# Optimization experiments

Measured on AMD Instinct MI355X. Metric: run time of the kernel, lower is better.

## Reference

```python
import jax, jax.numpy as jnp
import numpy as np

B, S, H = 8, 32, 2048          # batch, block (query) length, hidden size
NH, NKV, HD = 16, 2, 128       # attention heads, kv heads, head_dim
KV_LEN = 8192                  # block kv-cache length
GROUPS = NH // NKV
SCALE = HD ** -0.5


def rotate_half(x):
    x1, x2 = jnp.split(x, 2, axis=-1)
    return jnp.concatenate((-x2, x1), axis=-1)


def setup_inputs() -> dict:
    key = jax.random.key(0)
    ks = jax.random.split(key, 12)
    inv_freq = 1.0 / (10000.0 ** (jnp.arange(0, HD, 2, dtype=jnp.float32) / HD))
    pos = jnp.arange(S, dtype=jnp.float32)[:, None] * inv_freq[None, :]  # [S, HD/2]
    ang = jnp.concatenate([pos, pos], axis=-1)                           # [S, HD]
    cos = jnp.broadcast_to(jnp.cos(ang)[None], (B, S, HD))
    sin = jnp.broadcast_to(jnp.sin(ang)[None], (B, S, HD))
    s = 0.02
    return {
        'hidden_states': jax.random.normal(ks[0], (B, S, H), jnp.float32),
        'cos': cos,
        'sin': sin,
        'k_cache': jax.random.normal(ks[1], (B, NKV, KV_LEN, HD), jnp.float32),
        'v_cache': jax.random.normal(ks[2], (B, NKV, KV_LEN, HD), jnp.float32),
        'attention_mask': jnp.zeros((B, 1, S, KV_LEN), jnp.float32),
        'replace_position': 4096,
        'q_w': jax.random.normal(ks[3], (H, NH * HD), jnp.float32) * s,
        'q_b': jax.random.normal(ks[4], (NH * HD,), jnp.float32) * s,
        'k_w': jax.random.normal(ks[5], (H, NKV * HD), jnp.float32) * s,
        'k_b': jax.random.normal(ks[6], (NKV * HD,), jnp.float32) * s,
        'v_w': jax.random.normal(ks[7], (H, NKV * HD), jnp.float32) * s,
        'v_b': jax.random.normal(ks[8], (NKV * HD,), jnp.float32) * s,
        'o_w': jax.random.normal(ks[9], (NH * HD, H), jnp.float32) * s,
    }


def reference(hidden_states, cos, sin, k_cache, v_cache, attention_mask,
              replace_position, q_w, q_b, k_w, k_b, v_w, v_b, o_w):
    # fused QKV projections -> [B, heads, S, HD]
    q = (hidden_states @ q_w + q_b).reshape(B, S, NH, HD).transpose(0, 2, 1, 3)
    k = (hidden_states @ k_w + k_b).reshape(B, S, NKV, HD).transpose(0, 2, 1, 3)
    v = (hidden_states @ v_w + v_b).reshape(B, S, NKV, HD).transpose(0, 2, 1, 3)

    # RoPE (cos/sin unsqueezed on the head dim)
    c = cos[:, None]  # [B,1,S,HD]
    s_ = sin[:, None]
    q = q * c + rotate_half(q) * s_
    k = k * c + rotate_half(k) * s_

    # block KV-cache in-place update at replace_position
    k_all = jax.lax.dynamic_update_slice(k_cache, k, (0, 0, replace_position, 0))
    v_all = jax.lax.dynamic_update_slice(v_cache, v, (0, 0, replace_position, 0))

    # GQA: expand kv heads to match attention heads
    k_all = jnp.repeat(k_all, GROUPS, axis=1)  # [B,NH,KV,HD]
    v_all = jnp.repeat(v_all, GROUPS, axis=1)

    # SDPA with additive mask (is_causal=False)
    scores = jnp.einsum('bhqd,bhkd->bhqk', q, k_all) * SCALE + attention_mask
    probs = jax.nn.softmax(scores, axis=-1)
    attn = jnp.einsum('bhqk,bhkd->bhqd', probs, v_all)  # [B,NH,S,HD]

    out = attn.transpose(0, 2, 1, 3).reshape(B, S, NH * HD)
    return out @ o_w
```

## Files before the change

kernel.cpp:

```cpp
#include <hip/hip_runtime.h>
#include <hip/hip_bf16.h>

#define B_    8
#define S_    32
#define H_    2048
#define NH_   16
#define NKV_  2
#define HD_   128
#define KV_   8192
#define G_    8
#define M_    256
#define NQKV  2560
#define NSP   16
#define KT_   64
#define NT_   8
#define SCALE_ 0.08838834764831845f
#define CFIX_  8.0f
#define LOG2E_ 1.4426950408889634f
#define SCALE2_ (SCALE_*LOG2E_)

typedef __bf16 bf16x8 __attribute__((ext_vector_type(8)));
typedef float  f32x4  __attribute__((ext_vector_type(4)));
typedef float  f32x16 __attribute__((ext_vector_type(16)));

__device__ __forceinline__ unsigned short f2b(float f){
  unsigned u = __float_as_uint(f);
  u = u + 0x7FFFu + ((u>>16)&1u);
  return (unsigned short)(u>>16);
}
__device__ __forceinline__ float b2f(unsigned short h){
  return __uint_as_float(((unsigned)h)<<16);
}
__device__ __forceinline__ unsigned cvtpk(float lo, float hi){
  unsigned r;
  asm("v_cvt_pk_bf16_f32 %0, %1, %2" : "=v"(r) : "v"(lo), "v"(hi));
  return r;
}
__device__ __forceinline__ float fexp2(float x){
#if __has_builtin(__builtin_amdgcn_exp2f)
  return __builtin_amdgcn_exp2f(x);
#else
  return __expf(x * 0.6931471805599453f);
#endif
}
__device__ __forceinline__ bf16x8 ld_frag(const unsigned short* p){
  union { uint4 u; bf16x8 b; } cv;
  cv.u = *(const uint4*)p;
  return cv.b;
}
__device__ __forceinline__ f32x4 mf(bf16x8 a, bf16x8 b, f32x4 c){
  return __builtin_amdgcn_mfma_f32_16x16x32_bf16(a, b, c, 0, 0, 0);
}
__device__ __forceinline__ f32x16 mf32(bf16x8 a, bf16x8 b, f32x16 c){
  return __builtin_amdgcn_mfma_f32_32x32x16_bf16(a, b, c, 0, 0, 0);
}
__device__ __forceinline__ int swiK(int row, int col){
  return row*128 + (col ^ ((((row)&15) ^ ((row>>1)&8)) << 3));
}
__device__ __forceinline__ int swiV(int row, int col){
  return row*64 + (col ^ (((row)&7) << 3));
}

__global__ __launch_bounds__(256) void k_gemm_qkv(
    const float* __restrict__ A,
    const float* __restrict__ qw, const float* __restrict__ kw, const float* __restrict__ vw,
    const float* __restrict__ qbv, const float* __restrict__ kbv, const float* __restrict__ vbv,
    float* __restrict__ rawp)
{
  __shared__ unsigned short As[64][56];
  __shared__ unsigned short Bs[64][56];
  const int n0 = blockIdx.x*64, m0 = blockIdx.y*64, kz = blockIdx.z;
  const float* W; const float* bias; int ldw, wc0;
  if(n0 < 2048)      { W=qw; bias=qbv; ldw=2048; wc0=n0; }
  else if(n0 < 2304) { W=kw; bias=kbv; ldw=256;  wc0=n0-2048; }
  else               { W=vw; bias=vbv; ldw=256;  wc0=n0-2304; }
  const int t = threadIdx.x, lane = t&63, wid = t>>6;
  const int wr = wid>>1, wc = wid&1, l15 = lane&15, lq = lane>>4;
  const int ar = t>>2,  ac = (t&3)*8;
  const int bk = t>>5,  bn = (t&31)*2;
  f32x4 acc[2][2] = {};
  for(int k0 = kz*512; k0 < kz*512 + 512; k0 += 32){
    __syncthreads();
    { const float4 a0 = *(const float4*)(A + (m0+ar)*2048 + k0 + ac);
      const float4 a1 = *(const float4*)(A + (m0+ar)*2048 + k0 + ac + 4);
      uint4 w4; w4.x=cvtpk(a0.x,a0.y); w4.y=cvtpk(a0.z,a0.w);
                w4.z=cvtpk(a1.x,a1.y); w4.w=cvtpk(a1.z,a1.w);
      *(uint4*)(&As[ar][ac]) = w4; }
    #pragma unroll
    for(int p=0;p<4;p++){
      const int kk = bk + p*8;
      const float2 wv = *(const float2*)(W + (long)(k0+kk)*ldw + wc0 + bn);
      Bs[bn  ][kk] = f2b(wv.x);
      Bs[bn+1][kk] = f2b(wv.y);
    }
    __syncthreads();
    const bf16x8 a0 = ld_frag(&As[wr*32      + l15][lq*8]);
    const bf16x8 a1 = ld_frag(&As[wr*32 + 16 + l15][lq*8]);
    const bf16x8 b0 = ld_frag(&Bs[wc*32      + l15][lq*8]);
    const bf16x8 b1 = ld_frag(&Bs[wc*32 + 16 + l15][lq*8]);
    acc[0][0] = mf(a0,b0,acc[0][0]);
    acc[0][1] = mf(a0,b1,acc[0][1]);
    acc[1][0] = mf(a1,b0,acc[1][0]);
    acc[1][1] = mf(a1,b1,acc[1][1]);
  }
  float* out = rawp + (long)kz*M_*NQKV;
  #pragma unroll
  for(int mi=0;mi<2;mi++)
    #pragma unroll
    for(int nj=0;nj<2;nj++){
      const int col = n0 + wc*32 + nj*16 + l15;
      const float bv = kz ? 0.f : bias[wc0 + wc*32 + nj*16 + l15];
      #pragma unroll
      for(int rr=0;rr<4;rr++){
        const int row = m0 + wr*32 + mi*16 + lq*4 + rr;
        out[row*NQKV + col] = acc[mi][nj][rr] + bv;
      }
    }
}

__global__ __launch_bounds__(128) void k_rope(
    const float* __restrict__ rawp, const float* __restrict__ cosb, const float* __restrict__ sinb,
    unsigned short* __restrict__ Qb, float* __restrict__ KnF, float* __restrict__ VnF)
{
  const int r = blockIdx.x, hh = blockIdx.y, d = threadIdx.x;
  const int b = r>>5, s = r&31;
  const long MN = (long)M_*NQKV;
  const float cv = cosb[(b*S_+s)*HD_ + d];
  const float sv = sinb[(b*S_+s)*HD_ + d];
  const int dp = (d<64)? d+64 : d-64;
  #define RAW4(c) (rawp[r*NQKV+(c)] + rawp[MN+r*NQKV+(c)] + rawp[2*MN+r*NQKV+(c)] + rawp[3*MN+r*NQKV+(c)])
  if(hh < 16){
    const float x  = RAW4(hh*HD_ + d);
    const float xo = RAW4(hh*HD_ + dp);
    const float y  = x*cv + ((d<64)? -xo : xo)*sv;
    const int kvh = hh>>3, g = hh&7;
    Qb[((long)(b*NKV_+kvh)*M_ + g*S_ + s)*HD_ + d] = f2b(y);
  } else if(hh < 18){
    const int kvh = hh-16;
    const float x  = RAW4(2048 + kvh*HD_ + d);
    const float xo = RAW4(2048 + kvh*HD_ + dp);
    KnF[((long)(b*NKV_+kvh)*S_ + s)*HD_ + d] = x*cv + ((d<64)? -xo : xo)*sv;
  } else {
    const int kvh = hh-18;
    VnF[((long)(b*NKV_+kvh)*S_ + s)*HD_ + d] = RAW4(2304 + kvh*HD_ + d);
  }
  #undef RAW4
}

__global__ __launch_bounds__(256) void k_mswz(const float* __restrict__ mask,
                                              float* __restrict__ msw){
  const int g = blockIdx.x*256 + threadIdx.x;
  const int b = g >> 16, q = (g>>11)&31, c4 = g & 2047;
  const int kv = c4*4;
  const int sp = kv>>9, tt = (kv>>6)&7, kvt = (kv>>5)&1, r4 = (kv>>3)&3, hi = (kv>>2)&1;
  const int lane = q + 32*hi;
  float4 v = *(const float4*)(mask + ((long)b*S_ + q)*KV_ + kv);
  v.x = (v.x - CFIX_)*LOG2E_; v.y = (v.y - CFIX_)*LOG2E_;
  v.z = (v.z - CFIX_)*LOG2E_; v.w = (v.w - CFIX_)*LOG2E_;
  const long dst = ((((long)(b*NSP+sp)*NT_ + tt)*64 + lane)*8 + kvt*4 + r4);
  *(float4*)(msw + dst*4) = v;
}

__global__ __launch_bounds__(512, 2) void k_attn(
    const unsigned short* __restrict__ Qb,
    const float* __restrict__ KnF, const float* __restrict__ VnF,
    const float* __restrict__ kc, const float* __restrict__ vc,
    const float* __restrict__ msw, const int* __restrict__ rpp,
    unsigned short* __restrict__ num, float* __restrict__ lbuf)
{
  __shared__ __align__(16) unsigned short lds[2][2][KT_*128];
  const int sp = blockIdx.x, kvh = blockIdx.y, b = blockIdx.z;
  const int bk = b*NKV_ + kvh;
  const int rp = *rpp;
  const int t = threadIdx.x, lane = t&63, wid = t>>6;
  const int l31 = lane&31, hi = lane>>5;
  const int kvbase = sp*(KV_/NSP);
  const int krow = t>>3, kc0 = (t&7)*16;
  const int vhd  = t&127, vkq = t>>7;
  const int cbsK = (hi*8) ^ ((((l31)&15) ^ ((l31>>1)&8)) << 3);
  const int cbsV = (hi*8) ^ (((l31)&7) << 3);
  const int rowK = l31*128, rowV = l31*64;
  const int wk0 = swiK(krow, kc0), wk1 = swiK(krow, kc0+8);
  const int wv0 = swiV(vhd, vkq*16), wv1 = swiV(vhd, vkq*16+8);

  bf16x8 qf[8];
  { const unsigned short* qp = Qb + ((long)bk*M_ + wid*32 + l31)*HD_;
    #pragma unroll
    for(int ks=0;ks<8;ks++) qf[ks] = ld_frag(qp + ks*16 + hi*8); }

  float4 vK4[4];
  float  vV[16];
  float4 vM[8];
  const float4* mbase = (const float4*)msw + ((long)(b*NSP+sp)*NT_)*64*8 + lane*8;

  auto loadK = [&](int tt){
    const int kvr = kvbase + tt*KT_ + krow;
    const float* kp = (kvr>=rp && kvr<rp+S_)
        ? (KnF + ((long)bk*S_ + (kvr-rp))*HD_ + kc0)
        : (kc  + ((long)bk*KV_ + kvr)*HD_ + kc0);
    #pragma unroll
    for(int i=0;i<4;i++) vK4[i] = *(const float4*)(kp + i*4);
  };
  auto loadV = [&](int tt){
    #pragma unroll
    for(int m=0;m<16;m++){
      const int kvr = kvbase + tt*KT_ + vkq*16 + m;
      const float* vp = (kvr>=rp && kvr<rp+S_)
          ? (VnF + ((long)bk*S_ + (kvr-rp))*HD_)
          : (vc  + ((long)bk*KV_ + kvr)*HD_);
      vV[m] = vp[vhd];
    }
  };
  auto loadM = [&](int tt){
    const float4* mp = mbase + (long)tt*64*8;
    #pragma unroll
    for(int j=0;j<8;j++) vM[j] = mp[j];
  };
  auto writeK = [&](int bb){
    unsigned short* Sb = &lds[bb][0][0];
    uint4 w4;
    w4.x = cvtpk(vK4[0].x, vK4[0].y);  w4.y = cvtpk(vK4[0].z, vK4[0].w);
    w4.z = cvtpk(vK4[1].x, vK4[1].y);  w4.w = cvtpk(vK4[1].z, vK4[1].w);
    *(uint4*)(Sb + wk0) = w4;
    w4.x = cvtpk(vK4[2].x, vK4[2].y);  w4.y = cvtpk(vK4[2].z, vK4[2].w);
    w4.z = cvtpk(vK4[3].x, vK4[3].y);  w4.w = cvtpk(vK4[3].z, vK4[3].w);
    *(uint4*)(Sb + wk1) = w4;
  };
  auto writeV = [&](int bb){
    unsigned short* Sb = &lds[bb][1][0];
    uint4 w4;
    w4.x = cvtpk(vV[0], vV[1]);   w4.y = cvtpk(vV[2], vV[3]);
    w4.z = cvtpk(vV[4], vV[5]);   w4.w = cvtpk(vV[6], vV[7]);
    *(uint4*)(Sb + wv0) = w4;
    w4.x = cvtpk(vV[8], vV[9]);   w4.y = cvtpk(vV[10], vV[11]);
    w4.z = cvtpk(vV[12], vV[13]); w4.w = cvtpk(vV[14], vV[15]);
    *(uint4*)(Sb + wv1) = w4;
  };

  loadK(0); loadV(0);
  writeK(0); writeV(0);
  __syncthreads();

  f32x16 oc[4] = {};
  float l_run = 0.f;

  for(int tt=0; tt<NT_; tt++){
    const int cur = tt&1;
    loadM(tt);
    if(tt<NT_-1){ loadK(tt+1); loadV(tt+1); }
    f32x16 sc[2] = {};
    { const unsigned short* Sk = &lds[cur][0][0];
      __builtin_amdgcn_s_setprio(1);
      #pragma unroll
      for(int ks=0;ks<8;ks++){
        #pragma unroll
        for(int kvt=0;kvt<2;kvt++)
          sc[kvt] = mf32(ld_frag(Sk + rowK + kvt*4096 + (cbsK ^ (ks*16))), qf[ks], sc[kvt]);
      }
      __builtin_amdgcn_s_setprio(0);
    }
    float psum = 0.f;
    #pragma unroll
    for(int kvt=0;kvt<2;kvt++){
      #pragma unroll
      for(int r4=0;r4<4;r4++){
        const float4 mk = vM[kvt*4+r4];
        const float p0 = fexp2(fmaf(sc[kvt][r4*4+0], SCALE2_, mk.x));
        const float p1 = fexp2(fmaf(sc[kvt][r4*4+1], SCALE2_, mk.y));
        const float p2 = fexp2(fmaf(sc[kvt][r4*4+2], SCALE2_, mk.z));
        const float p3 = fexp2(fmaf(sc[kvt][r4*4+3], SCALE2_, mk.w));
        sc[kvt][r4*4+0]=p0; sc[kvt][r4*4+1]=p1;
        sc[kvt][r4*4+2]=p2; sc[kvt][r4*4+3]=p3;
        psum += (p0+p1)+(p2+p3);
      }
    }
    l_run += psum;
    unsigned w_[2][4][2];
    #pragma unroll
    for(int kvt=0;kvt<2;kvt++)
      #pragma unroll
      for(int r4=0;r4<4;r4++){
        w_[kvt][r4][0] = cvtpk(sc[kvt][r4*4+0], sc[kvt][r4*4+1]);
        w_[kvt][r4][1] = cvtpk(sc[kvt][r4*4+2], sc[kvt][r4*4+3]);
      }
    { const unsigned short* Sv = &lds[cur][1][0];
      __builtin_amdgcn_s_setprio(1);
      #pragma unroll
      for(int kvs=0;kvs<4;kvs++){
        const int kvt = kvs>>1, k2 = (kvs&1)*2;
        const unsigned wa0 = w_[kvt][k2  ][0], wa1 = w_[kvt][k2  ][1];
        const unsigned wb0 = w_[kvt][k2+1][0], wb1 = w_[kvt][k2+1][1];
        const unsigned own0 = hi? wb0:wa0, own1 = hi? wb1:wa1;
        const unsigned snd0 = hi? wa0:wb0, snd1 = hi? wa1:wb1;
        const unsigned rcv0 = __shfl_xor(snd0, 32, 64);
        const unsigned rcv1 = __shfl_xor(snd1, 32, 64);
        union{ unsigned u[4]; bf16x8 v; } ap;
        ap.u[0] = hi? rcv0:own0;  ap.u[1] = hi? rcv1:own1;
        ap.u[2] = hi? own0:rcv0;  ap.u[3] = hi? own1:rcv1;
        #pragma unroll
        for(int ht=0;ht<4;ht++)
          oc[ht] = mf32(ap.v, ld_frag(Sv + rowV + ht*2048 + (cbsV ^ (kvs*16))), oc[ht]);
      }
      __builtin_amdgcn_s_setprio(0);
    }
    if(tt<NT_-1){ writeK(cur^1); writeV(cur^1); }
    __syncthreads();
  }

  const float l_tot = l_run + __shfl_xor(l_run, 32, 64);
  if(lane < 32){
    lbuf[((long)bk*NSP + sp)*M_ + wid*32 + lane] = l_tot;
  }
  unsigned short* np_ = num + (((long)bk*NSP + sp)*M_ + wid*32)*HD_;
  #pragma unroll
  for(int ht=0;ht<4;ht++)
    #pragma unroll
    for(int r4=0;r4<4;r4++)
      #pragma unroll
      for(int rr=0;rr<4;rr++){
        const int q = rr + 8*r4 + 4*hi;
        np_[(long)q*HD_ + ht*32 + l31] = f2b(oc[ht][r4*4+rr]);
      }
}

__global__ __launch_bounds__(64) void k_comb(
    const unsigned short* __restrict__ num, const float* __restrict__ lbuf,
    unsigned short* __restrict__ attnb)
{
  const int q = blockIdx.x, kvh = blockIdx.y, b = blockIdx.z, d2 = threadIdx.x;
  const int bk = b*NKV_ + kvh;
  float den = 0.f, a0 = 0.f, a1 = 0.f;
  #pragma unroll
  for(int c=0;c<NSP;c++){
    const long ix = ((long)bk*NSP + c)*M_ + q;
    den += lbuf[ix];
    const unsigned u = *(const unsigned*)(num + ix*HD_ + 2*d2);
    a0 += b2f((unsigned short)(u & 0xffffu));
    a1 += b2f((unsigned short)(u >> 16));
  }
  const float r = 1.0f / den;
  const int g = q>>5, s = q&31, h = kvh*G_ + g;
  *(unsigned*)(attnb + ((long)(b*S_+s))*2048 + h*HD_ + 2*d2) = cvtpk(a0*r, a1*r);
}

__global__ __launch_bounds__(256) void k_gemm_o(
    const unsigned short* __restrict__ A,
    const float* __restrict__ W,
    float* __restrict__ owsp)
{
  __shared__ unsigned short As[64][56];
  __shared__ unsigned short Bs[64][56];
  const int n0 = blockIdx.x*64, m0 = blockIdx.y*64, kz = blockIdx.z;
  const int t = threadIdx.x, lane = t&63, wid = t>>6;
  const int wr = wid>>1, wc = wid&1, l15 = lane&15, lq = lane>>4;
  const int ar = t>>2,  ac = (t&3)*8;
  const int bk = t>>5,  bn = (t&31)*2;
  f32x4 acc[2][2] = {};
  for(int k0 = kz*512; k0 < kz*512 + 512; k0 += 32){
    __syncthreads();
    *(uint4*)(&As[ar][ac]) = *(const uint4*)(A + (m0+ar)*2048 + k0 + ac);
    #pragma unroll
    for(int p=0;p<4;p++){
      const int kk = bk + p*8;
      const float2 wv = *(const float2*)(W + (long)(k0+kk)*2048 + n0 + bn);
      Bs[bn  ][kk] = f2b(wv.x);
      Bs[bn+1][kk] = f2b(wv.y);
    }
    __syncthreads();
    const bf16x8 a0 = ld_frag(&As[wr*32      + l15][lq*8]);
    const bf16x8 a1 = ld_frag(&As[wr*32 + 16 + l15][lq*8]);
    const bf16x8 b0 = ld_frag(&Bs[wc*32      + l15][lq*8]);
    const bf16x8 b1 = ld_frag(&Bs[wc*32 + 16 + l15][lq*8]);
    acc[0][0] = mf(a0,b0,acc[0][0]);
    acc[0][1] = mf(a0,b1,acc[0][1]);
    acc[1][0] = mf(a1,b0,acc[1][0]);
    acc[1][1] = mf(a1,b1,acc[1][1]);
  }
  float* out = owsp + (long)kz*M_*2048;
  #pragma unroll
  for(int mi=0;mi<2;mi++)
    #pragma unroll
    for(int nj=0;nj<2;nj++){
      const int col = n0 + wc*32 + nj*16 + l15;
      #pragma unroll
      for(int rr=0;rr<4;rr++){
        const int row = m0 + wr*32 + mi*16 + lq*4 + rr;
        out[row*2048 + col] = acc[mi][nj][rr];
      }
    }
}

__global__ __launch_bounds__(256) void k_ored(const float* __restrict__ a,
                                              float* __restrict__ out){
  const int i = (blockIdx.x*256 + threadIdx.x)*4;
  const long MN = (long)M_*2048;
  const float4 x = *(const float4*)(a + i);
  const float4 y = *(const float4*)(a + MN + i);
  const float4 z = *(const float4*)(a + 2*MN + i);
  const float4 w = *(const float4*)(a + 3*MN + i);
  float4 o; o.x=(x.x+y.x)+(z.x+w.x); o.y=(x.y+y.y)+(z.y+w.y);
            o.z=(x.z+y.z)+(z.z+w.z); o.w=(x.w+y.w)+(z.w+w.w);
  *(float4*)(out + i) = o;
}

extern "C" void kernel_launch(void* const* d_in, const int* in_sizes, int n_in,
                              void* d_out, int out_size, void* d_ws, size_t ws_size,
                              hipStream_t stream){
  (void)in_sizes; (void)n_in; (void)out_size; (void)ws_size;
  const float* hs   = (const float*)d_in[0];
  const float* cosb = (const float*)d_in[1];
  const float* sinb = (const float*)d_in[2];
  const float* kc   = (const float*)d_in[3];
  const float* vc   = (const float*)d_in[4];
  const float* mask = (const float*)d_in[5];
  const int*   rp   = (const int*)  d_in[6];
  const float* qw   = (const float*)d_in[7];
  const float* qb   = (const float*)d_in[8];
  const float* kw   = (const float*)d_in[9];
  const float* kb   = (const float*)d_in[10];
  const float* vw   = (const float*)d_in[11];
  const float* vb   = (const float*)d_in[12];
  const float* ow   = (const float*)d_in[13];
  char* ws = (char*)d_ws;
  float*          rawp  = (float*)         (ws + 0);
  unsigned short* Qb    = (unsigned short*)(ws + 10485760);
  float*          KnF   = (float*)         (ws + 11534336);
  float*          VnF   = (float*)         (ws + 11796480);
  unsigned short* attnb = (unsigned short*)(ws + 12058624);
  float*          lbuf  = (float*)         (ws + 13107200);
  unsigned short* num   = (unsigned short*)(ws + 13369344);
  float*          owsp  = (float*)         (ws + 30146560);
  float*          msw   = (float*)         (ws + 38535168);
  float* outp = (float*)d_out;

  k_gemm_qkv<<<dim3(40,4,4),     dim3(256),  0, stream>>>(hs, qw,kw,vw, qb,kb,vb, rawp);
  k_mswz    <<<dim3(2048),       dim3(256),  0, stream>>>(mask, msw);
  k_rope    <<<dim3(256,20),     dim3(128),  0, stream>>>(rawp, cosb, sinb, Qb, KnF, VnF);
  k_attn    <<<dim3(NSP,2,8),    dim3(512),  0, stream>>>(Qb, KnF, VnF, kc, vc, msw, rp, num, lbuf);
  k_comb    <<<dim3(256,2,8),    dim3(64),   0, stream>>>(num, lbuf, attnb);
  k_gemm_o  <<<dim3(32,4,4),     dim3(256),  0, stream>>>(attnb, ow, owsp);
  k_ored    <<<dim3(512),        dim3(256),  0, stream>>>(owsp, outp);
}
```

Baseline: 98.11 us.

## Double-buffer GEMM tiles and fold mask swizzle into QKV GEMM launch

Both projection GEMMs now use double-buffered LDS tiles: the global loads for the next K-slice are issued before the MFMAs on the current slice, and there is one barrier per iteration instead of two. The mask-swizzle kernel is merged into the QKV GEMM launch as extra blocks (bx>=40), which removes one launch and lets mask preprocessing overlap with the GEMM. The cost is twice the LDS per block and more live registers for the prefetched data.

```diff
diff --git a/kernel.cpp b/kernel.cpp
--- a/kernel.cpp
+++ b/kernel.cpp
@@ -65,11 +65,28 @@
     const float* __restrict__ A,
     const float* __restrict__ qw, const float* __restrict__ kw, const float* __restrict__ vw,
     const float* __restrict__ qbv, const float* __restrict__ kbv, const float* __restrict__ vbv,
-    float* __restrict__ rawp)
+    float* __restrict__ rawp,
+    const float* __restrict__ mask, float* __restrict__ msw)
 {
-  __shared__ unsigned short As[64][56];
-  __shared__ unsigned short Bs[64][56];
-  const int n0 = blockIdx.x*64, m0 = blockIdx.y*64, kz = blockIdx.z;
+  __shared__ unsigned short As[2][64][56];
+  __shared__ unsigned short Bs[2][64][56];
+  const int bx = blockIdx.x;
+  if(bx >= 40){
+    const int mb = (bx-40) + 128*(blockIdx.y + 4*blockIdx.z);
+    const int g = mb*256 + threadIdx.x;
+    const int b = g >> 16, q = (g>>11)&31, c4 = g & 2047;
+    const int kv = c4*4;
+    const int sp = kv>>9, tt = (kv>>6)&7, kvt = (kv>>5)&1, r4 = (kv>>3)&3, hi = (kv>>2)&1;
+    const int lane = q + 32*hi;
+    float4 v = *(const float4*)(mask + ((long)b*S_ + q)*KV_ + kv);
+    v.x = (v.x - CFIX_)*LOG2E_; v.y = (v.y - CFIX_)*LOG2E_;
+    v.z = (v.z - CFIX_)*LOG2E_; v.w = (v.w - CFIX_)*LOG2E_;
+    const long dst = ((((long)(b*NSP+sp)*NT_ + tt)*64 + lane)*8 + kvt*4 + r4);
+    *(float4*)(msw + dst*4) = v;
+    return;
+  }
+  const int n0 = bx*64, m0 = blockIdx.y*64, kz = blockIdx.z;
+  const int kb = kz*512;
   const float* W; const float* bias; int ldw, wc0;
   if(n0 < 2048)      { W=qw; bias=qbv; ldw=2048; wc0=n0; }
   else if(n0 < 2304) { W=kw; bias=kbv; ldw=256;  wc0=n0-2048; }
@@ -78,30 +95,40 @@
   const int wr = wid>>1, wc = wid&1, l15 = lane&15, lq = lane>>4;
   const int ar = t>>2,  ac = (t&3)*8;
   const int bk = t>>5,  bn = (t&31)*2;
+  float4 a0r, a1r; float2 wvr[4];
+  auto loadAB = [&](int k0){
+    a0r = *(const float4*)(A + (m0+ar)*2048 + k0 + ac);
+    a1r = *(const float4*)(A + (m0+ar)*2048 + k0 + ac + 4);
+    #pragma unroll
+    for(int p=0;p<4;p++)
+      wvr[p] = *(const float2*)(W + (long)(k0 + bk + p*8)*ldw + wc0 + bn);
+  };
+  auto writeAB = [&](int buf){
+    uint4 w4; w4.x=cvtpk(a0r.x,a0r.y); w4.y=cvtpk(a0r.z,a0r.w);
+              w4.z=cvtpk(a1r.x,a1r.y); w4.w=cvtpk(a1r.z,a1r.w);
+    *(uint4*)(&As[buf][ar][ac]) = w4;
+    #pragma unroll
+    for(int p=0;p<4;p++){
+      Bs[buf][bn  ][bk+p*8] = f2b(wvr[p].x);
+      Bs[buf][bn+1][bk+p*8] = f2b(wvr[p].y);
+    }
+  };
+  loadAB(kb); writeAB(0);
+  __syncthreads();
   f32x4 acc[2][2] = {};
-  for(int k0 = kz*512; k0 < kz*512 + 512; k0 += 32){
-    __syncthreads();
-    { const float4 a0 = *(const float4*)(A + (m0+ar)*2048 + k0 + ac);
-      const float4 a1 = *(const float4*)(A + (m0+ar)*2048 + k0 + ac + 4);
-      uint4 w4; w4.x=cvtpk(a0.x,a0.y); w4.y=cvtpk(a0.z,a0.w);
-                w4.z=cvtpk(a1.x,a1.y); w4.w=cvtpk(a1.z,a1.w);
-      *(uint4*)(&As[ar][ac]) = w4; }
-    #pragma unroll
-    for(int p=0;p<4;p++){
-      const int kk = bk + p*8;
-      const float2 wv = *(const float2*)(W + (long)(k0+kk)*ldw + wc0 + bn);
-      Bs[bn  ][kk] = f2b(wv.x);
-      Bs[bn+1][kk] = f2b(wv.y);
-    }
-    __syncthreads();
-    const bf16x8 a0 = ld_frag(&As[wr*32      + l15][lq*8]);
-    const bf16x8 a1 = ld_frag(&As[wr*32 + 16 + l15][lq*8]);
-    const bf16x8 b0 = ld_frag(&Bs[wc*32      + l15][lq*8]);
-    const bf16x8 b1 = ld_frag(&Bs[wc*32 + 16 + l15][lq*8]);
+  for(int i=0;i<16;i++){
+    const int cur = i&1;
+    if(i<15) loadAB(kb + (i+1)*32);
+    const bf16x8 a0 = ld_frag(&As[cur][wr*32      + l15][lq*8]);
+    const bf16x8 a1 = ld_frag(&As[cur][wr*32 + 16 + l15][lq*8]);
+    const bf16x8 b0 = ld_frag(&Bs[cur][wc*32      + l15][lq*8]);
+    const bf16x8 b1 = ld_frag(&Bs[cur][wc*32 + 16 + l15][lq*8]);
     acc[0][0] = mf(a0,b0,acc[0][0]);
     acc[0][1] = mf(a0,b1,acc[0][1]);
     acc[1][0] = mf(a1,b0,acc[1][0]);
     acc[1][1] = mf(a1,b1,acc[1][1]);
+    if(i<15) writeAB(cur^1);
+    __syncthreads();
   }
   float* out = rawp + (long)kz*M_*NQKV;
   #pragma unroll
@@ -147,20 +174,6 @@
   #undef RAW4
 }
 
-__global__ __launch_bounds__(256) void k_mswz(const float* __restrict__ mask,
-                                              float* __restrict__ msw){
-  const int g = blockIdx.x*256 + threadIdx.x;
-  const int b = g >> 16, q = (g>>11)&31, c4 = g & 2047;
-  const int kv = c4*4;
-  const int sp = kv>>9, tt = (kv>>6)&7, kvt = (kv>>5)&1, r4 = (kv>>3)&3, hi = (kv>>2)&1;
-  const int lane = q + 32*hi;
-  float4 v = *(const float4*)(mask + ((long)b*S_ + q)*KV_ + kv);
-  v.x = (v.x - CFIX_)*LOG2E_; v.y = (v.y - CFIX_)*LOG2E_;
-  v.z = (v.z - CFIX_)*LOG2E_; v.w = (v.w - CFIX_)*LOG2E_;
-  const long dst = ((((long)(b*NSP+sp)*NT_ + tt)*64 + lane)*8 + kvt*4 + r4);
-  *(float4*)(msw + dst*4) = v;
-}
-
 __global__ __launch_bounds__(512, 2) void k_attn(
     const unsigned short* __restrict__ Qb,
     const float* __restrict__ KnF, const float* __restrict__ VnF,
@@ -348,33 +361,45 @@
     const float* __restrict__ W,
     float* __restrict__ owsp)
 {
-  __shared__ unsigned short As[64][56];
-  __shared__ unsigned short Bs[64][56];
+  __shared__ unsigned short As[2][64][56];
+  __shared__ unsigned short Bs[2][64][56];
   const int n0 = blockIdx.x*64, m0 = blockIdx.y*64, kz = blockIdx.z;
+  const int kb = kz*512;
   const int t = threadIdx.x, lane = t&63, wid = t>>6;
   const int wr = wid>>1, wc = wid&1, l15 = lane&15, lq = lane>>4;
   const int ar = t>>2,  ac = (t&3)*8;
   const int bk = t>>5,  bn = (t&31)*2;
+  uint4 a4r; float2 wvr[4];
+  auto loadAB = [&](int k0){
+    a4r = *(const uint4*)(A + (m0+ar)*2048 + k0 + ac);
+    #pragma unroll
+    for(int p=0;p<4;p++)
+      wvr[p] = *(const float2*)(W + (long)(k0 + bk + p*8)*2048 + n0 + bn);
+  };
+  auto writeAB = [&](int buf){
+    *(uint4*)(&As[buf][ar][ac]) = a4r;
+    #pragma unroll
+    for(int p=0;p<4;p++){
+      Bs[buf][bn  ][bk+p*8] = f2b(wvr[p].x);
+      Bs[buf][bn+1][bk+p*8] = f2b(wvr[p].y);
+    }
+  };
+  loadAB(kb); writeAB(0);
+  __syncthreads();
   f32x4 acc[2][2] = {};
-  for(int k0 = kz*512; k0 < kz*512 + 512; k0 += 32){
-    __syncthreads();
-    *(uint4*)(&As[ar][ac]) = *(const uint4*)(A + (m0+ar)*2048 + k0 + ac);
-    #pragma unroll
-    for(int p=0;p<4;p++){
-      const int kk = bk + p*8;
-      const float2 wv = *(const float2*)(W + (long)(k0+kk)*2048 + n0 + bn);
-      Bs[bn  ][kk] = f2b(wv.x);
-      Bs[bn+1][kk] = f2b(wv.y);
-    }
-    __syncthreads();
-    const bf16x8 a0 = ld_frag(&As[wr*32      + l15][lq*8]);
-    const bf16x8 a1 = ld_frag(&As[wr*32 + 16 + l15][lq*8]);
-    const bf16x8 b0 = ld_frag(&Bs[wc*32      + l15][lq*8]);
-    const bf16x8 b1 = ld_frag(&Bs[wc*32 + 16 + l15][lq*8]);
+  for(int i=0;i<16;i++){
+    const int cur = i&1;
+    if(i<15) loadAB(kb + (i+1)*32);
+    const bf16x8 a0 = ld_frag(&As[cur][wr*32      + l15][lq*8]);
+    const bf16x8 a1 = ld_frag(&As[cur][wr*32 + 16 + l15][lq*8]);
+    const bf16x8 b0 = ld_frag(&Bs[cur][wc*32      + l15][lq*8]);
+    const bf16x8 b1 = ld_frag(&Bs[cur][wc*32 + 16 + l15][lq*8]);
     acc[0][0] = mf(a0,b0,acc[0][0]);
     acc[0][1] = mf(a0,b1,acc[0][1]);
     acc[1][0] = mf(a1,b0,acc[1][0]);
     acc[1][1] = mf(a1,b1,acc[1][1]);
+    if(i<15) writeAB(cur^1);
+    __syncthreads();
   }
   float* out = owsp + (long)kz*M_*2048;
   #pragma unroll
@@ -433,8 +458,7 @@
   float*          msw   = (float*)         (ws + 38535168);
   float* outp = (float*)d_out;
 
-  k_gemm_qkv<<<dim3(40,4,4),     dim3(256),  0, stream>>>(hs, qw,kw,vw, qb,kb,vb, rawp);
-  k_mswz    <<<dim3(2048),       dim3(256),  0, stream>>>(mask, msw);
+  k_gemm_qkv<<<dim3(168,4,4),    dim3(256),  0, stream>>>(hs, qw,kw,vw, qb,kb,vb, rawp, mask, msw);
   k_rope    <<<dim3(256,20),     dim3(128),  0, stream>>>(rawp, cosb, sinb, Qb, KnF, VnF);
   k_attn    <<<dim3(NSP,2,8),    dim3(512),  0, stream>>>(Qb, KnF, VnF, kc, vc, msw, rp, num, lbuf);
   k_comb    <<<dim3(256,2,8),    dim3(64),   0, stream>>>(num, lbuf, attnb);
```

New measurement: 101.5 us. +3.4%, slower.
